# Kernel tuning notes

Hardware: AMD Instinct MI355X
Metric: run time of the kernel (lower is better)

## Reference

```python
import jax, jax.numpy as jnp
import numpy as np
from jax import lax

S = 2048      # services
MAXL = 16     # max exec steps per service
D = 4096      # devices
RN = 128      # size_realnode
HN = 128      # size_hypernode
HEADS = 4
CH = RN + HN  # 256
NRO = 256     # readout neurons
NITER = 3
NEG = 0.2     # leaky relu slope


def _gru(x, h, Wih, Whh, bih, bhh):
    # PyTorch GRU/GRUCell equations, gate order (r, z, n)
    gi = x @ Wih + bih
    gh = h @ Whh + bhh
    ir, iz, ig = jnp.split(gi, 3, axis=-1)
    hr, hz, hg = jnp.split(gh, 3, axis=-1)
    r = jax.nn.sigmoid(ir + hr)
    z = jax.nn.sigmoid(iz + hz)
    n = jnp.tanh(ig + r * hg)
    return (1.0 - z) * n + z * h


def _mlp(x, W1, b1, W2, b2, W3, b3):
    # Linear-ReLU-(Dropout eval=id)-Linear-ReLU-Linear
    h = jax.nn.relu(x @ W1 + b1)
    h = jax.nn.relu(h @ W2 + b2)
    return h @ W3 + b3


def forward(realnode, arr, exeSeqs, index_devices, index_fragments, frag2dev_node, frag2dev_row, lengths, frag_service, frag_pos,
            W_dev, b_dev, W_frg, b_frg, W_srv, b_srv,
            C_Wih, C_Whh, C_bih, C_bhh, F_Wih, F_Whh, F_bih, F_bhh, D_Wih, D_Whh, D_bih, D_bhh,
            W_src, b_src, W_tgt, b_tgt, att, bias_att,
            Wt1, bt1, Wt2, bt2, Wt3, bt3, Wl1, bl1, Wl2, bl2, Wl3, bl3):
    nodes = realnode.shape[0] + 1          # row 0 is zero-pad row (1-based node ids)
    Sn, L2 = exeSeqs.shape
    L = L2 // 2
    Dn = index_devices.shape[0]
    dtype = realnode.dtype

    # initial real-node states (scatter with disjoint indices == set)
    devs = realnode[index_devices - 1] @ W_dev + b_dev
    frags = realnode[index_fragments - 1] @ W_frg + b_frg
    state = jnp.zeros((nodes, RN), dtype).at[index_devices].set(devs).at[index_fragments].set(frags)

    h_srv = arr @ W_srv + b_srv            # [S, HN] GRU hidden (torch shape [1,S,HN])
    frag_state = state[index_fragments]

    for _ in range(NITER):
        # phiC: packed GRU over per-service execution sequences
        seq = state[exeSeqs].reshape(Sn, L, 2 * RN)   # [S, L, 2*RN]

        def step(h, xt_t):
            xt, t = xt_t
            hn = _gru(xt, h, C_Wih, C_Whh, C_bih, C_bhh)
            h = jnp.where((t < lengths)[:, None], hn, h)  # packed semantics: freeze past length
            return h, h

        h_srv, outs = lax.scan(step, h_srv, (seq.transpose(1, 0, 2), jnp.arange(L)))
        outs = outs.transpose(1, 0, 2)                # [S, L, HN]
        out_f = outs[frag_service, frag_pos]          # [F, HN] valid steps only (extract_indices)

        # messageF: hypernode output || state of device hosting the fragment
        msgF = jnp.concatenate([out_f, state[frag2dev_node]], axis=-1)   # [F, HN+RN]
        frag_state = state[index_fragments]
        frag_old = frag_state
        frag_state = _gru(msgF, frag_state, F_Wih, F_Whh, F_bih, F_bhh)

        # GAT-style scatter softmax over devices
        src = (jnp.concatenate([out_f, frag_old], axis=-1) @ W_src + b_src).reshape(-1, HEADS, CH)  # [F,H,CH]
        dev_state = state[index_devices]
        tgt = (dev_state @ W_tgt + b_tgt).reshape(-1, HEADS, CH)                                    # [D,H,CH]
        e = jax.nn.leaky_relu(src + tgt[frag2dev_row], NEG)
        alpha = (e * att).sum(-1)                                        # [F, HEADS]
        amax = jax.ops.segment_max(alpha, frag2dev_row, num_segments=Dn)
        w = jnp.exp(alpha - amax[frag2dev_row])
        wsum = jax.ops.segment_sum(w, frag2dev_row, num_segments=Dn)
        a = w / (wsum[frag2dev_row] + 1e-16)
        msgD = jax.ops.segment_sum(src * a[:, :, None], frag2dev_row, num_segments=Dn)
        msgD = msgD.mean(axis=1) + bias_att                              # [D, CH]
        dev_state = _gru(msgD, dev_state, D_Wih, D_Whh, D_bih, D_bhh)

        state = jnp.zeros((nodes, RN), dtype).at[index_devices].set(dev_state).at[index_fragments].set(frag_state)

    # mean-pool fragment states per service
    pooled = jax.ops.segment_sum(frag_state, frag_service, num_segments=Sn) / lengths[:, None].astype(dtype)
    latency = _mlp(pooled, Wl1, bl1, Wl2, bl2, Wl3, bl3)[:, 0]           # [S]
    thr = _mlp(h_srv, Wt1, bt1, Wt2, bt2, Wt3, bt3)[:, 0]                # [S]
    return jnp.concatenate([latency, thr])[None, :]                      # [1, 2S]


def setup_inputs() -> dict:
    lengths_np = np.tile(np.array([4, 8, 12, 16], dtype=np.int64), S // 4)
    F = int(lengths_np.sum())            # 20480 fragments
    num_real = D + F                     # 24576
    rng = np.random.RandomState(0)
    frag2dev_row = rng.randint(0, D, size=F).astype(np.int64)       # device row per fragment
    frag_service = np.repeat(np.arange(S, dtype=np.int64), lengths_np)
    frag_pos = np.concatenate([np.arange(l, dtype=np.int64) for l in lengths_np])
    index_devices = np.arange(1, D + 1, dtype=np.int64)             # 1-based node ids
    index_fragments = np.arange(D + 1, D + F + 1, dtype=np.int64)
    dev_node = frag2dev_row + 1
    exeSeqs = np.zeros((S, 2 * MAXL), dtype=np.int64)               # pad with 0 (zero row)
    exeSeqs[frag_service, 2 * frag_pos] = index_fragments
    exeSeqs[frag_service, 2 * frag_pos + 1] = dev_node

    keys = iter(jax.random.split(jax.random.key(0), 64))
    def rn(shape, s=0.05):
        return jax.random.normal(next(keys), shape, jnp.float32) * s
    z = lambda *sh: jnp.zeros(sh, jnp.float32)

    return {
        'realnode': rn((num_real, 5), 1.0), 'arr': rn((S, 5), 1.0),
        'exeSeqs': jnp.asarray(exeSeqs), 'index_devices': jnp.asarray(index_devices),
        'index_fragments': jnp.asarray(index_fragments), 'frag2dev_node': jnp.asarray(dev_node),
        'frag2dev_row': jnp.asarray(frag2dev_row), 'lengths': jnp.asarray(lengths_np),
        'frag_service': jnp.asarray(frag_service), 'frag_pos': jnp.asarray(frag_pos),
        'W_dev': rn((5, RN), 0.3), 'b_dev': z(RN), 'W_frg': rn((5, RN), 0.3), 'b_frg': z(RN),
        'W_srv': rn((5, HN), 0.3), 'b_srv': z(HN),
        'C_Wih': rn((2 * RN, 3 * HN)), 'C_Whh': rn((HN, 3 * HN)), 'C_bih': z(3 * HN), 'C_bhh': z(3 * HN),
        'F_Wih': rn((CH, 3 * RN)), 'F_Whh': rn((RN, 3 * RN)), 'F_bih': z(3 * RN), 'F_bhh': z(3 * RN),
        'D_Wih': rn((CH, 3 * RN)), 'D_Whh': rn((RN, 3 * RN)), 'D_bih': z(3 * RN), 'D_bhh': z(3 * RN),
        'W_src': rn((CH, HEADS * CH)), 'b_src': z(HEADS * CH),
        'W_tgt': rn((RN, HEADS * CH)), 'b_tgt': z(HEADS * CH),
        'att': rn((1, HEADS, CH), 0.1), 'bias_att': z(CH),
        'Wt1': rn((HN, NRO)), 'bt1': z(NRO), 'Wt2': rn((NRO, NRO)), 'bt2': z(NRO), 'Wt3': rn((NRO, 1)), 'bt3': z(1),
        'Wl1': rn((RN, NRO)), 'bl1': z(NRO), 'Wl2': rn((NRO, NRO)), 'bl2': z(NRO), 'Wl3': rn((NRO, 1)), 'bl3': z(1),
    }


def reference(realnode, arr, exeSeqs, index_devices, index_fragments, frag2dev_node, frag2dev_row, lengths, frag_service, frag_pos,
              W_dev, b_dev, W_frg, b_frg, W_srv, b_srv,
              C_Wih, C_Whh, C_bih, C_bhh, F_Wih, F_Whh, F_bih, F_bhh, D_Wih, D_Whh, D_bih, D_bhh,
              W_src, b_src, W_tgt, b_tgt, att, bias_att,
              Wt1, bt1, Wt2, bt2, Wt3, bt3, Wl1, bl1, Wl2, bl2, Wl3, bl3):
    return forward(realnode, arr, exeSeqs, index_devices, index_fragments, frag2dev_node, frag2dev_row, lengths, frag_service, frag_pos,
                   W_dev, b_dev, W_frg, b_frg, W_srv, b_srv,
                   C_Wih, C_Whh, C_bih, C_bhh, F_Wih, F_Whh, F_bih, F_bhh, D_Wih, D_Whh, D_bih, D_bhh,
                   W_src, b_src, W_tgt, b_tgt, att, bias_att,
                   Wt1, bt1, Wt2, bt2, Wt3, bt3, Wl1, bl1, Wl2, bl2, Wl3, bl3)
```

## Files before the change

kernel.cpp:

```cpp
#include <hip/hip_runtime.h>
#include <hip/hip_bf16.h>

typedef __attribute__((ext_vector_type(8))) short bf16x8;
typedef __attribute__((ext_vector_type(4))) float f32x4;

__device__ __forceinline__ float sigf(float x){ return 1.0f/(1.0f+expf(-x)); }
__device__ __forceinline__ int clampi(int v, int lo, int hi){ return v<lo?lo:(v>hi?hi:v); }
__device__ __forceinline__ unsigned short f2b(float f){
    __hip_bfloat16 h = __float2bfloat16(f);
    return *reinterpret_cast<unsigned short*>(&h);
}
__device__ __forceinline__ float us2f(unsigned short u){ return __uint_as_float(((unsigned)u)<<16); }

__device__ __forceinline__ void gload16(const void* g, void* l){
    __builtin_amdgcn_global_load_lds((const __attribute__((address_space(1))) void*)g,
                                     (__attribute__((address_space(3))) void*)l, 16, 0, 0);
}

__global__ void k_cvt(const int* __restrict__ src, int* __restrict__ dst, int n,
                      const int* __restrict__ det)
{
    int i = blockIdx.x*blockDim.x + threadIdx.x;
    if (i >= n) return;
    int stride = (det[1] == 0) ? 2 : 1;
    dst[i] = src[(size_t)i*stride];
}

__global__ void k_wt(const float* __restrict__ W, unsigned short* __restrict__ Wt,
                     int N, int kshift, int kmask, int total)
{
    int idx = blockIdx.x*blockDim.x + threadIdx.x;
    if (idx >= total) return;
    int n = idx >> kshift, k = idx & kmask;
    Wt[idx] = f2b(W[(size_t)k*N + n]);
}

__global__ void k_wt2(const float* __restrict__ W, unsigned short* __restrict__ Whi,
                      unsigned short* __restrict__ Wlo, int N, int kshift, int kmask, int total)
{
    int idx = blockIdx.x*blockDim.x + threadIdx.x;
    if (idx >= total) return;
    int n = idx >> kshift, k = idx & kmask;
    float v = W[(size_t)k*N + n];
    unsigned short hi = f2b(v);
    Whi[idx] = hi;
    Wlo[idx] = f2b(v - us2f(hi));
}

__global__ void k_proj5(const float* __restrict__ X, const float* __restrict__ W,
                        const float* __restrict__ bias,
                        const int* __restrict__ gidx, const int* __restrict__ sidx,
                        float* __restrict__ out, unsigned short* __restrict__ outBf,
                        float* __restrict__ out2, unsigned short* __restrict__ out2Bf,
                        int M, int nrows, int nodes)
{
    int t = blockIdx.x*blockDim.x + threadIdx.x;
    int i = t >> 7, j = t & 127;
    if (i >= M) return;
    int src = gidx ? clampi(gidx[i]-1, 0, nrows-1) : i;
    const float* xp = X + (size_t)src*5;
    float acc = bias[j];
#pragma unroll
    for (int k=0;k<5;k++) acc += xp[k] * W[k*128+j];
    int dr = sidx ? clampi(sidx[i], 0, nodes-1) : i;
    if (out)   out[(size_t)dr*128 + j] = acc;
    if (outBf) outBf[(size_t)dr*128 + j] = f2b(acc);
    if (out2)  out2[(size_t)i*128 + j] = acc;
    if (out2Bf) out2Bf[(size_t)i*128 + j] = f2b(acc);
}

__launch_bounds__(256)
__global__ void k_mm(const float* __restrict__ A0, int lda,
                     const float* __restrict__ B, int ldb,
                     const float* __restrict__ bias, float* __restrict__ C,
                     int M, int N, int K, int relu, float scale, int accum)
{
    __shared__ float As[16][132];
    __shared__ float Bs[16][132];
    int tid = threadIdx.x;
    int tx = tid & 15, ty = tid >> 4;
    int row0 = blockIdx.y * 128, col0 = blockIdx.x * 128;
    float acc[8][8] = {};
    for (int k0 = 0; k0 < K; k0 += 16){
#pragma unroll
        for (int q = 0; q < 2; ++q){
            int idx = tid + q*256;
            int r = idx >> 2, k4 = (idx & 3) * 4;
            const float* src = A0 + (size_t)(row0+r)*lda + k0 + k4;
            float4 v = *reinterpret_cast<const float4*>(src);
            As[k4+0][r]=v.x; As[k4+1][r]=v.y; As[k4+2][r]=v.z; As[k4+3][r]=v.w;
        }
#pragma unroll
        for (int q = 0; q < 2; ++q){
            int idx = tid + q*256;
            int kb = idx >> 5, n4 = (idx & 31) * 4;
            float4 v = *reinterpret_cast<const float4*>(B + (size_t)(k0+kb)*ldb + col0 + n4);
            *reinterpret_cast<float4*>(&Bs[kb][n4]) = v;
        }
        __syncthreads();
#pragma unroll
        for (int k = 0; k < 16; ++k){
            float a[8], b[8];
            *(float4*)&a[0] = *(const float4*)&As[k][ty*8];
            *(float4*)&a[4] = *(const float4*)&As[k][ty*8+4];
            *(float4*)&b[0] = *(const float4*)&Bs[k][tx*8];
            *(float4*)&b[4] = *(const float4*)&Bs[k][tx*8+4];
#pragma unroll
            for (int i=0;i<8;i++)
#pragma unroll
                for (int j=0;j<8;j++) acc[i][j] += a[i]*b[j];
        }
        __syncthreads();
    }
    float bb[8];
#pragma unroll
    for (int j=0;j<8;j++) bb[j] = bias ? bias[col0+tx*8+j] : 0.f;
#pragma unroll
    for (int i=0;i<8;i++){
        float* cp = C + (size_t)(row0+ty*8+i)*N + col0 + tx*8;
#pragma unroll
        for (int jq=0;jq<2;jq++){
            float4 prev = accum ? *(const float4*)(cp+jq*4) : make_float4(0,0,0,0);
            float o[4];
#pragma unroll
            for (int c=0;c<4;c++){
                float u = acc[i][jq*4+c] + bb[jq*4+c];
                if (relu) u = fmaxf(u,0.f);
                o[c] = (&prev.x)[c] + scale*u;
            }
            *(float4*)(cp+jq*4) = make_float4(o[0],o[1],o[2],o[3]);
        }
    }
}

struct MJob {
    const unsigned short *A0, *A1;
    const int *i0, *i1;
    const unsigned short *Wt;
    const float *bias;
    void *C;
    int N, K, epi, nrow;
    float scale;
};

#define MM2_SMEM 67840

__device__ __forceinline__ void mm2_body(const MJob J, int bid, char* smem)
{
    unsigned short* AsB = (unsigned short*)smem;
    unsigned short* BsB = AsB + 16384;
    int tid = threadIdx.x;
    int l = tid & 63, w = tid >> 6;
    int wr = w >> 1, wc = w & 1;
    int row0 = (bid % J.nrow) * 128, col0 = (bid / J.nrow) * 128;
    int nK = J.K >> 6;

    f32x4 acc[4][4];
#pragma unroll
    for (int m=0;m<4;m++)
#pragma unroll
        for (int n=0;n<4;n++) acc[m][n] = (f32x4){0.f,0.f,0.f,0.f};

    auto stage = [&](int buf, int k0){
        unsigned short* As = AsB + buf*8192;
        unsigned short* Bs = BsB + buf*8192;
#pragma unroll
        for (int q=0;q<4;q++){
            int slot = q*256 + w*64 + l;
            int r = slot >> 3, c8 = slot & 7;
            int g8 = c8 ^ (r & 7);
            int row; const unsigned short* base; int kl;
            if (k0 < 128){ row = J.i0 ? J.i0[row0+r] : (row0+r); base = J.A0; kl = k0; }
            else         { row = J.i1 ? J.i1[row0+r] : (row0+r); base = J.A1; kl = k0-128; }
            const char* g = (const char*)(base + (size_t)row*128 + kl) + g8*16;
            gload16(g, (void*)&As[(size_t)(q*256 + w*64)*8]);
        }
#pragma unroll
        for (int q=0;q<4;q++){
            int slot = q*256 + w*64 + l;
            int n = slot >> 3, kc = slot & 7;
            int g8 = kc ^ (n & 7);
            const char* g = (const char*)(J.Wt + (size_t)(col0+n)*J.K + k0) + g8*16;
            gload16(g, (void*)&Bs[(size_t)(q*256 + w*64)*8]);
        }
    };

    stage(0, 0);
    __syncthreads();
    for (int ks=0; ks<nK; ++ks){
        int cur = ks & 1;
        if (ks+1 < nK) stage(cur^1, (ks+1)*64);
        unsigned short* As = AsB + cur*8192;
        unsigned short* Bs = BsB + cur*8192;
#pragma unroll
        for (int kk = 0; kk < 2; ++kk){
            int ek = kk*32 + (l >> 4) * 8;
            bf16x8 af[4], bf[4];
#pragma unroll
            for (int m=0;m<4;m++){
                int r = wr*64 + m*16 + (l & 15);
                af[m] = *reinterpret_cast<const bf16x8*>(&As[r*64 + (ek ^ ((r & 7) << 3))]);
            }
#pragma unroll
            for (int n=0;n<4;n++){
                int c = wc*64 + n*16 + (l & 15);
                bf[n] = *reinterpret_cast<const bf16x8*>(&Bs[c*64 + (ek ^ ((c & 7) << 3))]);
            }
#pragma unroll
            for (int m=0;m<4;m++)
#pragma unroll
                for (int n=0;n<4;n++)
                    acc[m][n] = __builtin_amdgcn_mfma_f32_16x16x32_bf16(af[m], bf[n], acc[m][n], 0, 0, 0);
        }
        __syncthreads();
    }

    if (J.epi == 0){
        float* Ct = (float*)smem;
#pragma unroll
        for (int m=0;m<4;m++){
#pragma unroll
            for (int v=0;v<4;v++){
                int rl = wr*64 + m*16 + (l >> 4)*4 + v;
#pragma unroll
                for (int n=0;n<4;n++){
                    int c = wc*64 + n*16 + (l & 15);
                    Ct[rl*132 + c] = J.scale*acc[m][n][v] + (J.bias ? J.bias[col0+c] : 0.f);
                }
            }
        }
        __syncthreads();
#pragma unroll
        for (int q=0;q<16;q++){
            int idx = tid + q*256;
            int r = idx >> 5, c4 = (idx & 31)*4;
            float4 v = *reinterpret_cast<const float4*>(&Ct[r*132 + c4]);
            *reinterpret_cast<float4*>((float*)J.C + (size_t)(row0+r)*J.N + col0 + c4) = v;
        }
    } else {
        unsigned short* Cb = (unsigned short*)smem;
#pragma unroll
        for (int m=0;m<4;m++){
#pragma unroll
            for (int v=0;v<4;v++){
                int rl = wr*64 + m*16 + (l >> 4)*4 + v;
#pragma unroll
                for (int n=0;n<4;n++){
                    int c = wc*64 + n*16 + (l & 15);
                    Cb[rl*136 + c] = f2b(J.scale*acc[m][n][v] + (J.bias ? J.bias[col0+c] : 0.f));
                }
            }
        }
        __syncthreads();
#pragma unroll
        for (int q=0;q<8;q++){
            int idx = tid + q*256;
            int r = idx >> 4, c8 = (idx & 15)*8;
            uint4 v = *reinterpret_cast<const uint4*>(&Cb[r*136 + c8]);
            *reinterpret_cast<uint4*>((unsigned short*)J.C + (size_t)(row0+r)*J.N + col0 + c8) = v;
        }
    }
}

__launch_bounds__(256)
__global__ void mm2one(MJob a)
{
    __shared__ alignas(16) char smem[MM2_SMEM];
    mm2_body(a, blockIdx.x, smem);
}

__launch_bounds__(256)
__global__ void mm2two(MJob a, MJob b, int asplit)
{
    __shared__ alignas(16) char smem[MM2_SMEM];
    int bid = blockIdx.x;
    if (bid < asplit) mm2_body(a, bid, smem);
    else              mm2_body(b, bid - asplit, smem);
}

struct GJob {
    const unsigned short *A0, *A1;
    const int *i0, *i1;
    int lda;
    const unsigned short *Wih, *Whh;
    const float *bih, *bhh;
    float *H;
    unsigned short *Hbf, *stateBf;
    const int *sidx;
    int M, nodes;
};

__device__ __forceinline__ void gru_body(const GJob J, int bid, unsigned short* AsB, unsigned short* BsB)
{
    int tid = threadIdx.x;
    int l = tid & 63, w = tid >> 6;
    int row0 = bid * 128;
    f32x4 acc[24], accN[8];
#pragma unroll
    for (int n=0;n<24;n++) acc[n] = (f32x4){0.f,0.f,0.f,0.f};
#pragma unroll
    for (int n=0;n<8;n++) accN[n] = (f32x4){0.f,0.f,0.f,0.f};

    auto stage = [&](int buf, int st){
        int k0 = st*64;
        unsigned short* As = AsB + buf*8192;
        unsigned short* Bs = BsB + buf*24576;
#pragma unroll
        for (int q=0;q<2;q++){
            int slot = q*512 + w*64 + l;
            int r = slot >> 3, c8 = slot & 7;
            int g8 = c8 ^ (r & 7);
            const unsigned short* src;
            if (st < 4){
                if (J.i1){
                    if (k0 < 128){ int ri = J.i0 ? J.i0[row0+r] : (row0+r); src = J.A0 + (size_t)ri*128 + k0; }
                    else         { int ri = J.i1[row0+r]; src = J.A1 + (size_t)ri*128 + (k0-128); }
                } else {
                    src = J.A0 + (size_t)(row0+r)*J.lda + k0;
                }
            } else {
                src = J.Hbf + (size_t)(row0+r)*128 + (k0-256);
            }
            gload16((const char*)src + g8*16, (void*)&As[(size_t)(q*512 + w*64)*8]);
        }
#pragma unroll
        for (int q=0;q<6;q++){
            int slot = q*512 + w*64 + l;
            int n = slot >> 3, kc = slot & 7;
            int g8 = kc ^ (n & 7);
            const unsigned short* src = (st < 4) ? (J.Wih + (size_t)n*256 + k0)
                                                 : (J.Whh + (size_t)n*128 + (k0-256));
            gload16((const char*)src + g8*16, (void*)&Bs[(size_t)(q*512 + w*64)*8]);
        }
    };

    stage(0, 0);
    __syncthreads();
    for (int st=0; st<4; ++st){
        int cur = st & 1;
        stage(cur^1, st+1);
        unsigned short* As = AsB + cur*8192;
        unsigned short* Bs = BsB + cur*24576;
#pragma unroll
        for (int kk=0; kk<2; ++kk){
            int ek = kk*32 + (l >> 4)*8;
            int r = w*16 + (l & 15);
            bf16x8 af = *reinterpret_cast<const bf16x8*>(&As[r*64 + (ek ^ ((r & 7) << 3))]);
#pragma unroll
            for (int n=0;n<24;n++){
                int c = n*16 + (l & 15);
                bf16x8 bf = *reinterpret_cast<const bf16x8*>(&Bs[c*64 + (ek ^ ((c & 7) << 3))]);
                acc[n] = __builtin_amdgcn_mfma_f32_16x16x32_bf16(af, bf, acc[n], 0, 0, 0);
            }
        }
        __syncthreads();
    }
    for (int st=4; st<6; ++st){
        int cur = st & 1;
        if (st+1 < 6) stage(cur^1, st+1);
        unsigned short* As = AsB + cur*8192;
        unsigned short* Bs = BsB + cur*24576;
#pragma unroll
        for (int kk=0; kk<2; ++kk){
            int ek = kk*32 + (l >> 4)*8;
            int r = w*16 + (l & 15);
            bf16x8 af = *reinterpret_cast<const bf16x8*>(&As[r*64 + (ek ^ ((r & 7) << 3))]);
#pragma unroll
            for (int n=0;n<24;n++){
                int c = n*16 + (l & 15);
                bf16x8 bf = *reinterpret_cast<const bf16x8*>(&Bs[c*64 + (ek ^ ((c & 7) << 3))]);
                if (n < 16) acc[n]     = __builtin_amdgcn_mfma_f32_16x16x32_bf16(af, bf, acc[n], 0, 0, 0);
                else        accN[n-16] = __builtin_amdgcn_mfma_f32_16x16x32_bf16(af, bf, accN[n-16], 0, 0, 0);
            }
        }
        __syncthreads();
    }
#pragma unroll
    for (int v=0;v<4;v++){
        int row = row0 + w*16 + (l >> 4)*4 + v;
        int st = clampi(J.sidx[row],0,J.nodes-1);
#pragma unroll
        for (int c=0;c<8;c++){
            int col = c*16 + (l & 15);
            float rr = sigf(acc[c][v]    + J.bih[col]     + J.bhh[col]);
            float zz = sigf(acc[c+8][v]  + J.bih[col+128] + J.bhh[col+128]);
            float nn = tanhf(acc[c+16][v] + J.bih[col+256] + rr*(accN[c][v] + J.bhh[col+256]));
            float hv = J.H[(size_t)row*128 + col];
            float hn = (1.f-zz)*nn + zz*hv;
            unsigned short hb = f2b(hn);
            J.H[(size_t)row*128 + col] = hn;
            J.Hbf[(size_t)row*128 + col] = hb;
            J.stateBf[(size_t)st*128 + col] = hb;
        }
    }
}

__launch_bounds__(512)
__global__ void gru2(GJob a, GJob b, int asplit)
{
    __shared__ alignas(16) unsigned short AsB[2*8192];
    __shared__ alignas(16) unsigned short BsB[2*24576];
    int bid = blockIdx.x;
    if (bid < asplit) gru_body(a, bid, AsB, BsB);
    else              gru_body(b, bid - asplit, AsB, BsB);
}

__launch_bounds__(256)
__global__ void k_attn(const unsigned short* __restrict__ SRC, const unsigned short* __restrict__ tgtbf,
                       const float* __restrict__ att, const int* __restrict__ list,
                       const int* __restrict__ offs, const float* __restrict__ batt,
                       unsigned short* __restrict__ msgDbf,
                       float* __restrict__ alphaG, int Dn, int F)
{
    __shared__ float tg[1024];
    __shared__ float alds[128*4];
    __shared__ float accs[4][256];
    int d = blockIdx.x;
    int tid = threadIdx.x;
    int w = tid >> 6, lane = tid & 63;
    for (int u = tid; u < 1024; u += 256) tg[u] = us2f(tgtbf[(size_t)d*1024 + u]);
    __syncthreads();
    int beg = offs[d], end = offs[d+1];
    if (beg < 0) beg = 0; if (end > F) end = F; if (end < beg) end = beg;
    int c0 = w*256 + lane*4;
    float t0 = tg[c0], t1 = tg[c0+1], t2 = tg[c0+2], t3 = tg[c0+3];
    float a0 = att[c0], a1 = att[c0+1], a2 = att[c0+2], a3 = att[c0+3];
    float amax = -3.4e38f;
    for (int i=beg;i<end;i++){
        int f = list[i];
        ushort4 sv = *reinterpret_cast<const ushort4*>(SRC + (size_t)f*1024 + c0);
        float e0 = us2f(sv.x)+t0, e1 = us2f(sv.y)+t1, e2 = us2f(sv.z)+t2, e3 = us2f(sv.w)+t3;
        e0 = e0>0.f?e0:0.2f*e0; e1 = e1>0.f?e1:0.2f*e1;
        e2 = e2>0.f?e2:0.2f*e2; e3 = e3>0.f?e3:0.2f*e3;
        float s = e0*a0 + e1*a1 + e2*a2 + e3*a3;
#pragma unroll
        for (int msk=1; msk<64; msk<<=1) s += __shfl_xor(s, msk);
        int li = i - beg;
        if (li < 128){ if (lane == 0) alds[li*4+w] = s; }
        else         { if (lane == 0) alphaG[(size_t)f*4+w] = s; }
        amax = fmaxf(amax, s);
    }
    __syncthreads();
    float wsum = 0.f;
    for (int i=beg;i<end;i++){
        int li = i - beg;
        float a = (li < 128) ? alds[li*4+w] : alphaG[(size_t)list[i]*4+w];
        wsum += expf(a - amax);
    }
    float iws = 1.f/(wsum + 1e-16f);
    float acc[4] = {0,0,0,0};
    for (int i=beg;i<end;i++){
        int f = list[i];
        int li = i - beg;
        float a = (li < 128) ? alds[li*4+w] : alphaG[(size_t)f*4+w];
        float p = expf(a - amax)*iws;
        ushort4 sv = *reinterpret_cast<const ushort4*>(SRC + (size_t)f*1024 + c0);
        acc[0] += p*us2f(sv.x); acc[1] += p*us2f(sv.y);
        acc[2] += p*us2f(sv.z); acc[3] += p*us2f(sv.w);
    }
#pragma unroll
    for (int j=0;j<4;j++) accs[w][lane*4+j] = acc[j];
    __syncthreads();
    if (tid < 256){
        float m = (accs[0][tid]+accs[1][tid]+accs[2][tid]+accs[3][tid])*0.25f + batt[tid];
        msgDbf[(size_t)d*256 + tid] = f2b(m);
    }
}

__launch_bounds__(512)
__global__ void k_recur(float* __restrict__ h_srv, const float* __restrict__ giF,
                        const unsigned short* __restrict__ Whi,
                        const unsigned short* __restrict__ Wlo,
                        const float* __restrict__ bhh,
                        const int* __restrict__ inv,
                        unsigned short* __restrict__ out_f_bf,
                        int S, int L, int F)
{
    __shared__ float hs[16][129];
    __shared__ alignas(16) unsigned short hsHi[16*128];
    __shared__ alignas(16) unsigned short hsLo[16*128];
    __shared__ float ghs[16][385];
    __shared__ int fLoc[16][16];
    int tid = threadIdx.x;
    int l = tid & 63, w = tid >> 6;
    int lane15 = l & 15, lhi = l >> 4;
    int s0 = blockIdx.x * 16;
    for (int u = tid; u < 2048; u += 512){
        int s=u>>7,k=u&127;
        float v = h_srv[(size_t)(s0+s)*128+k];
        hs[s][k] = v;
        unsigned short hb = f2b(v);
        int ksw = k ^ ((s & 7) << 3);
        hsHi[s*128 + ksw] = hb;
        hsLo[s*128 + ksw] = f2b(v - us2f(hb));
    }
    if (tid < 256) fLoc[tid>>4][tid&15] = inv[(size_t)(s0+(tid&15))*L + (tid>>4)];
    bf16x8 wHi[3][4], wLo[3][4];
#pragma unroll
    for (int ct=0; ct<3; ++ct){
        int col = w*48 + ct*16 + lane15;
#pragma unroll
        for (int ks=0; ks<4; ++ks){
            size_t off = (size_t)col*128 + ks*32 + lhi*8;
            wHi[ct][ks] = *reinterpret_cast<const bf16x8*>(Whi + off);
            wLo[ct][ks] = *reinterpret_cast<const bf16x8*>(Wlo + off);
        }
    }
    __syncthreads();
    for (int t=0;t<L;++t){
        bf16x8 hHi[4], hLo[4];
#pragma unroll
        for (int ks=0; ks<4; ++ks){
            int ek = ks*32 + lhi*8;
            int off = lane15*128 + (ek ^ ((lane15 & 7) << 3));
            hHi[ks] = *reinterpret_cast<const bf16x8*>(&hsHi[off]);
            hLo[ks] = *reinterpret_cast<const bf16x8*>(&hsLo[off]);
        }
#pragma unroll
        for (int ct=0; ct<3; ++ct){
            f32x4 acc = (f32x4){0.f,0.f,0.f,0.f};
#pragma unroll
            for (int ks=0; ks<4; ++ks){
                acc = __builtin_amdgcn_mfma_f32_16x16x32_bf16(hHi[ks], wHi[ct][ks], acc, 0,0,0);
                acc = __builtin_amdgcn_mfma_f32_16x16x32_bf16(hLo[ks], wHi[ct][ks], acc, 0,0,0);
                acc = __builtin_amdgcn_mfma_f32_16x16x32_bf16(hHi[ks], wLo[ct][ks], acc, 0,0,0);
            }
            int col = w*48 + ct*16 + lane15;
            float bb = bhh[col];
#pragma unroll
            for (int v=0; v<4; ++v){
                ghs[lhi*4 + v][col] = acc[v] + bb;
            }
        }
        __syncthreads();
        for (int u = tid; u < 2048; u += 512){
            int s=u>>7, k=u&127; int f = fLoc[t][s];
            if (f >= 0 && f < F){
                const float* gp = giF + (size_t)f*384;
                float r  = sigf(gp[k]     + ghs[s][k]);
                float zz = sigf(gp[128+k] + ghs[s][128+k]);
                float n  = tanhf(gp[256+k] + r*ghs[s][256+k]);
                float hn = (1.f-zz)*n + zz*hs[s][k];
                hs[s][k] = hn;
                unsigned short hb = f2b(hn);
                int ksw = k ^ ((s & 7) << 3);
                hsHi[s*128 + ksw] = hb;
                hsLo[s*128 + ksw] = f2b(hn - us2f(hb));
                out_f_bf[(size_t)f*128+k] = hb;
            }
        }
        __syncthreads();
    }
    for (int u = tid; u < 2048; u += 512){ int s=u>>7,k=u&127; h_srv[(size_t)(s0+s)*128+k] = hs[s][k]; }
}

__global__ void k_count(const int* __restrict__ row, int* __restrict__ counts, int F, int Dn)
{ int f = blockIdx.x*blockDim.x + threadIdx.x; if (f < F) atomicAdd(&counts[clampi(row[f],0,Dn-1)], 1); }

__global__ void k_scan(const int* __restrict__ counts, int* __restrict__ offs, int D)
{
    __shared__ int part[257];
    int tid = threadIdx.x;
    int per = (D + 255) / 256;
    int s = 0;
    for (int i=0;i<per;i++){ int idx = tid*per+i; if (idx < D) s += counts[idx]; }
    part[tid] = s;
    __syncthreads();
    if (tid == 0){
        int acc = 0;
        for (int i=0;i<256;i++){ int v = part[i]; part[i] = acc; acc += v; }
        part[256] = acc;
    }
    __syncthreads();
    int acc = part[tid];
    for (int i=0;i<per;i++){ int idx = tid*per+i; if (idx < D){ offs[idx] = acc; acc += counts[idx]; } }
    if (tid == 0) offs[D] = part[256];
}

__global__ void k_fill(const int* __restrict__ row, const int* __restrict__ offs,
                       int* __restrict__ cursor, int* __restrict__ list, int F, int Dn)
{
    int f = blockIdx.x*blockDim.x + threadIdx.x;
    if (f >= F) return;
    int r = clampi(row[f],0,Dn-1);
    int p = atomicAdd(&cursor[r], 1);
    int pos = offs[r]+p;
    if (pos >= 0 && pos < F) list[pos] = f;
}

__global__ void k_build_inv(const int* __restrict__ fs, const int* __restrict__ fp,
                            int* __restrict__ inv, int F, int L, int S)
{
    int f = blockIdx.x*blockDim.x + threadIdx.x;
    if (f >= F) return;
    inv[clampi(fs[f],0,S-1)*L + clampi(fp[f],0,L-1)] = f;
}

__global__ void k_pool_add(const float* __restrict__ frag, const int* __restrict__ fs,
                           float* __restrict__ pooled, int F, int S)
{
    int t = blockIdx.x*blockDim.x + threadIdx.x;
    int i = t >> 7, j = t & 127;
    if (i >= F) return;
    atomicAdd(&pooled[(size_t)clampi(fs[i],0,S-1)*128 + j], frag[(size_t)i*128 + j]);
}

__global__ void k_pool_div(float* __restrict__ pooled, const int* __restrict__ lengths, int S)
{
    int t = blockIdx.x*blockDim.x + threadIdx.x;
    int i = t >> 7, j = t & 127;
    if (i >= S) return;
    int l = lengths[i]; if (l < 1) l = 1;
    pooled[(size_t)i*128 + j] /= (float)l;
}

__global__ void k_dot_out(const float* __restrict__ H, const float* __restrict__ W3,
                          const float* __restrict__ b3, float* __restrict__ outv, int off)
{
    __shared__ float red[256];
    int s = blockIdx.x, tid = threadIdx.x;
    red[tid] = H[(size_t)s*256 + tid] * W3[tid];
    __syncthreads();
    for (int st=128; st; st>>=1){ if (tid < st) red[tid] += red[tid+st]; __syncthreads(); }
    if (tid == 0) outv[off + s] = red[0] + b3[0];
}

extern "C" void kernel_launch(void* const* d_in, const int* in_sizes, int n_in,
                              void* d_out, int out_size, void* d_ws, size_t ws_size,
                              hipStream_t stream)
{
    (void)n_in; (void)out_size; (void)ws_size;
    const float* realnode = (const float*)d_in[0];
    const float* arr      = (const float*)d_in[1];
    const int* r_exe   = (const int*)d_in[2];
    const int* r_idev  = (const int*)d_in[3];
    const int* r_ifrag = (const int*)d_in[4];
    const int* r_fdn   = (const int*)d_in[5];
    const int* r_fdr   = (const int*)d_in[6];
    const int* r_len   = (const int*)d_in[7];
    const int* r_fsvc  = (const int*)d_in[8];
    const int* r_fpos  = (const int*)d_in[9];
    const float *W_dev=(const float*)d_in[10], *b_dev=(const float*)d_in[11];
    const float *W_frg=(const float*)d_in[12], *b_frg=(const float*)d_in[13];
    const float *W_srv=(const float*)d_in[14], *b_srv=(const float*)d_in[15];
    const float *C_Wih=(const float*)d_in[16], *C_Whh=(const float*)d_in[17], *C_bih=(const float*)d_in[18], *C_bhh=(const float*)d_in[19];
    const float *F_Wih=(const float*)d_in[20], *F_Whh=(const float*)d_in[21], *F_bih=(const float*)d_in[22], *F_bhh=(const float*)d_in[23];
    const float *D_Wih=(const float*)d_in[24], *D_Whh=(const float*)d_in[25], *D_bih=(const float*)d_in[26], *D_bhh=(const float*)d_in[27];
    const float *W_src=(const float*)d_in[28], *b_src=(const float*)d_in[29];
    const float *W_tgt=(const float*)d_in[30], *b_tgt=(const float*)d_in[31];
    const float *att=(const float*)d_in[32], *bias_att=(const float*)d_in[33];
    const float *Wt1=(const float*)d_in[34], *bt1=(const float*)d_in[35], *Wt2=(const float*)d_in[36], *bt2=(const float*)d_in[37], *Wt3=(const float*)d_in[38], *bt3=(const float*)d_in[39];
    const float *Wl1=(const float*)d_in[40], *bl1=(const float*)d_in[41], *Wl2=(const float*)d_in[42], *bl2=(const float*)d_in[43], *Wl3=(const float*)d_in[44], *bl3=(const float*)d_in[45];
    float* outp = (float*)d_out;

    const int S  = in_sizes[7];
    const int Dn = in_sizes[3];
    const int F  = in_sizes[4];
    const int L  = in_sizes[2] / (2*S);
    const int nreal = in_sizes[0]/5;
    const int nodes = nreal + 1;
    const int NIT = 3;

    char* wp = (char*)d_ws;
    auto alloc = [&](size_t nelem)->float*{
        float* p = (float*)wp;
        wp += ((nelem*4 + 255)/256)*256;
        return p;
    };
    float* h_srv  = alloc((size_t)S*128);
    float* fragA  = alloc((size_t)F*128);
    float* devA   = alloc((size_t)Dn*128);
    float* alphaB = alloc((size_t)F*4);
    float* UNION  = alloc((size_t)F*512);
    float* giF    = UNION;
    unsigned short* SRC = (unsigned short*)UNION;
    float* Z      = alloc((size_t)Dn*1024);
    float* TGTf   = alloc((size_t)Dn*512);
    unsigned short* TGT = (unsigned short*)TGTf;
    float* pooled = alloc((size_t)S*128);
    unsigned short* state_bf = (unsigned short*)alloc((size_t)nodes*64);
    unsigned short* out_f_bf = (unsigned short*)alloc((size_t)F*64);
    unsigned short* fragA_bf = (unsigned short*)alloc((size_t)F*64);
    unsigned short* devA_bf  = (unsigned short*)alloc((size_t)Dn*64);
    unsigned short* msgD_bf  = (unsigned short*)alloc((size_t)Dn*128);
    unsigned short* tCWih   = (unsigned short*)alloc(384*256/2);
    unsigned short* tCWhhHi = (unsigned short*)alloc(384*128/2);
    unsigned short* tCWhhLo = (unsigned short*)alloc(384*128/2);
    unsigned short* tFWih   = (unsigned short*)alloc(384*256/2);
    unsigned short* tFWhh   = (unsigned short*)alloc(384*128/2);
    unsigned short* tDWih   = (unsigned short*)alloc(384*256/2);
    unsigned short* tDWhh   = (unsigned short*)alloc(384*128/2);
    unsigned short* tWtgt   = (unsigned short*)alloc(1024*128/2);
    unsigned short* tWsrc   = (unsigned short*)alloc(1024*256/2);
    int* cExe   = (int*)alloc((size_t)S*2*L);
    int* cIdev  = (int*)alloc((size_t)Dn);
    int* cIfrag = (int*)alloc((size_t)F);
    int* cFdn   = (int*)alloc((size_t)F);
    int* cFdr   = (int*)alloc((size_t)F);
    int* cLen   = (int*)alloc((size_t)S);
    int* cFsvc  = (int*)alloc((size_t)F);
    int* cFpos  = (int*)alloc((size_t)F);
    int* inv    = (int*)alloc((size_t)S*L);
    int* counts = (int*)alloc((size_t)Dn);
    int* offs   = (int*)alloc((size_t)Dn+1);
    int* cursor = (int*)alloc((size_t)Dn);
    int* list   = (int*)alloc((size_t)F);

    const int* det = r_idev;
    auto cvt = [&](const int* src, int* dst, int n){
        k_cvt<<<dim3((n+255)/256),256,0,stream>>>(src, dst, n, det);
    };
    cvt(r_exe,  cExe,  S*2*L);
    cvt(r_idev, cIdev, Dn);
    cvt(r_ifrag,cIfrag,F);
    cvt(r_fdn,  cFdn,  F);
    cvt(r_fdr,  cFdr,  F);
    cvt(r_len,  cLen,  S);
    cvt(r_fsvc, cFsvc, F);
    cvt(r_fpos, cFpos, F);

    k_wt<<<dim3((98304+255)/256),256,0,stream>>>(C_Wih, tCWih, 384, 8, 255, 98304);
    k_wt2<<<dim3((49152+255)/256),256,0,stream>>>(C_Whh, tCWhhHi, tCWhhLo, 384, 7, 127, 49152);
    k_wt<<<dim3((98304+255)/256),256,0,stream>>>(F_Wih, tFWih, 384, 8, 255, 98304);
    k_wt<<<dim3((49152+255)/256),256,0,stream>>>(F_Whh, tFWhh, 384, 7, 127, 49152);
    k_wt<<<dim3((98304+255)/256),256,0,stream>>>(D_Wih, tDWih, 384, 8, 255, 98304);
    k_wt<<<dim3((49152+255)/256),256,0,stream>>>(D_Whh, tDWhh, 384, 7, 127, 49152);
    k_wt<<<dim3((131072+255)/256),256,0,stream>>>(W_tgt, tWtgt, 1024, 7, 127, 131072);
    k_wt<<<dim3((262144+255)/256),256,0,stream>>>(W_src, tWsrc, 1024, 8, 255, 262144);

    hipMemsetAsync(state_bf, 0, (size_t)nodes*128*2, stream);
    hipMemsetAsync(inv, 0xFF, (size_t)S*L*4, stream);
    hipMemsetAsync(counts, 0, (size_t)Dn*4, stream);
    hipMemsetAsync(cursor, 0, (size_t)Dn*4, stream);

    k_proj5<<<dim3((Dn*128+255)/256),256,0,stream>>>(realnode, W_dev, b_dev, cIdev, cIdev,
        nullptr, state_bf, devA, devA_bf, Dn, nreal, nodes);
    k_proj5<<<dim3(((size_t)F*128+255)/256),256,0,stream>>>(realnode, W_frg, b_frg, cIfrag, cIfrag,
        nullptr, state_bf, fragA, fragA_bf, F, nreal, nodes);
    k_proj5<<<dim3((S*128+255)/256),256,0,stream>>>(arr, W_srv, b_srv, nullptr, nullptr,
        h_srv, nullptr, nullptr, nullptr, S, S, nodes);
    k_build_inv<<<dim3((F+255)/256),256,0,stream>>>(cFsvc, cFpos, inv, F, L, S);
    k_count<<<dim3((F+255)/256),256,0,stream>>>(cFdr, counts, F, Dn);
    k_scan<<<1,256,0,stream>>>(counts, offs, Dn);
    k_fill<<<dim3((F+255)/256),256,0,stream>>>(cFdr, offs, cursor, list, F, Dn);

    const int nrF = F/128, nrD = Dn/128;
    MJob jGi  = { state_bf, state_bf, cIfrag, cFdn, tCWih, C_bih, giF, 384, 256, 0, nrF, 1.f };
    MJob jTgt = { devA_bf, devA_bf, nullptr, nullptr, tWtgt, b_tgt, TGT, 1024, 128, 2, nrD, 1.f };
    MJob jSrc = { out_f_bf, fragA_bf, nullptr, nullptr, tWsrc, b_src, SRC, 1024, 256, 2, nrF, 1.f };
    GJob jF = { out_f_bf, state_bf, nullptr, cFdn, 128, tFWih, tFWhh, F_bih, F_bhh,
                fragA, fragA_bf, state_bf, cIfrag, F, nodes };
    GJob jD = { msgD_bf, nullptr, nullptr, nullptr, 256, tDWih, tDWhh, D_bih, D_bhh,
                devA, devA_bf, state_bf, cIdev, Dn, nodes };

    for (int it=0; it<NIT; ++it){
        mm2two<<<dim3(3*nrF + 8*nrD),256,0,stream>>>(jGi, jTgt, 3*nrF);
        k_recur<<<dim3(S/16),512,0,stream>>>(h_srv, giF, tCWhhHi, tCWhhLo, C_bhh, inv,
            out_f_bf, S, L, F);
        mm2one<<<dim3(8*nrF),256,0,stream>>>(jSrc);
        k_attn<<<dim3(Dn),256,0,stream>>>(SRC, TGT, att, list, offs, bias_att,
            msgD_bf, alphaB, Dn, F);
        gru2<<<dim3(nrF + nrD),512,0,stream>>>(jF, jD, nrF);
    }

    hipMemsetAsync(pooled, 0, (size_t)S*128*4, stream);
    k_pool_add<<<dim3(((size_t)F*128+255)/256),256,0,stream>>>(fragA, cFsvc, pooled, F, S);
    k_pool_div<<<dim3((S*128+255)/256),256,0,stream>>>(pooled, cLen, S);
    float* h1 = (float*)TGTf;
    k_mm<<<dim3(256/128, S/128),256,0,stream>>>(pooled, 128, Wl1, 256, bl1, h1, S, 256, 128, 1, 1.f, 0);
    k_mm<<<dim3(256/128, S/128),256,0,stream>>>(h1, 256, Wl2, 256, bl2, Z, S, 256, 256, 1, 1.f, 0);
    k_dot_out<<<dim3(S),256,0,stream>>>(Z, Wl3, bl3, outp, 0);
    k_mm<<<dim3(256/128, S/128),256,0,stream>>>(h_srv, 128, Wt1, 256, bt1, h1, S, 256, 128, 1, 1.f, 0);
    k_mm<<<dim3(256/128, S/128),256,0,stream>>>(h1, 256, Wt2, 256, bt2, Z, S, 256, 256, 1, 1.f, 0);
    k_dot_out<<<dim3(S),256,0,stream>>>(Z, Wt3, bt3, outp, S);
}
```

Before: 859.6 us.

## Pipeline GEMM staging with partial vmcnt waits, halve recur block size, bf16 gi

The GEMM and GRU kernels now use explicit s_waitcnt vmcnt with raw barriers instead of __syncthreads, so the next stage's async LDS loads can stay in flight while the current tile is computed. The two GRU stage loops are merged into one. The recurrent kernel handles 8 services per block instead of 16, doubling the grid for the sequential scan. The gi projection is stored in bf16, which halves its memory traffic at some cost in precision. The vmcnt(8) count assumes a fixed number of outstanding loads per stage, and half of the padded MFMA rows in k_recur now do no useful work.

```diff
diff --git a/kernel.cpp b/kernel.cpp
--- a/kernel.cpp
+++ b/kernel.cpp
@@ -186,10 +186,16 @@
     };
 
     stage(0, 0);
-    __syncthreads();
     for (int ks=0; ks<nK; ++ks){
         int cur = ks & 1;
-        if (ks+1 < nK) stage(cur^1, (ks+1)*64);
+        if (ks+1 < nK){
+            stage(cur^1, (ks+1)*64);
+            asm volatile("s_waitcnt vmcnt(8)" ::: "memory");
+        } else {
+            asm volatile("s_waitcnt vmcnt(0)" ::: "memory");
+        }
+        __builtin_amdgcn_s_barrier();
+        __builtin_amdgcn_sched_barrier(0);
         unsigned short* As = AsB + cur*8192;
         unsigned short* Bs = BsB + cur*8192;
 #pragma unroll
@@ -212,7 +218,8 @@
                 for (int n=0;n<4;n++)
                     acc[m][n] = __builtin_amdgcn_mfma_f32_16x16x32_bf16(af[m], bf[n], acc[m][n], 0, 0, 0);
         }
-        __syncthreads();
+        __builtin_amdgcn_sched_barrier(0);
+        __builtin_amdgcn_s_barrier();
     }
 
     if (J.epi == 0){
@@ -335,45 +342,48 @@
     };
 
     stage(0, 0);
-    __syncthreads();
-    for (int st=0; st<4; ++st){
+    for (int st=0; st<6; ++st){
         int cur = st & 1;
-        stage(cur^1, st+1);
+        if (st+1 < 6){
+            stage(cur^1, st+1);
+            asm volatile("s_waitcnt vmcnt(8)" ::: "memory");
+        } else {
+            asm volatile("s_waitcnt vmcnt(0)" ::: "memory");
+        }
+        __builtin_amdgcn_s_barrier();
+        __builtin_amdgcn_sched_barrier(0);
         unsigned short* As = AsB + cur*8192;
         unsigned short* Bs = BsB + cur*24576;
-#pragma unroll
-        for (int kk=0; kk<2; ++kk){
-            int ek = kk*32 + (l >> 4)*8;
-            int r = w*16 + (l & 15);
-            bf16x8 af = *reinterpret_cast<const bf16x8*>(&As[r*64 + (ek ^ ((r & 7) << 3))]);
-#pragma unroll
-            for (int n=0;n<24;n++){
-                int c = n*16 + (l & 15);
-                bf16x8 bf = *reinterpret_cast<const bf16x8*>(&Bs[c*64 + (ek ^ ((c & 7) << 3))]);
-                acc[n] = __builtin_amdgcn_mfma_f32_16x16x32_bf16(af, bf, acc[n], 0, 0, 0);
-            }
-        }
-        __syncthreads();
-    }
-    for (int st=4; st<6; ++st){
-        int cur = st & 1;
-        if (st+1 < 6) stage(cur^1, st+1);
-        unsigned short* As = AsB + cur*8192;
-        unsigned short* Bs = BsB + cur*24576;
-#pragma unroll
-        for (int kk=0; kk<2; ++kk){
-            int ek = kk*32 + (l >> 4)*8;
-            int r = w*16 + (l & 15);
-            bf16x8 af = *reinterpret_cast<const bf16x8*>(&As[r*64 + (ek ^ ((r & 7) << 3))]);
-#pragma unroll
-            for (int n=0;n<24;n++){
-                int c = n*16 + (l & 15);
-                bf16x8 bf = *reinterpret_cast<const bf16x8*>(&Bs[c*64 + (ek ^ ((c & 7) << 3))]);
-                if (n < 16) acc[n]     = __builtin_amdgcn_mfma_f32_16x16x32_bf16(af, bf, acc[n], 0, 0, 0);
-                else        accN[n-16] = __builtin_amdgcn_mfma_f32_16x16x32_bf16(af, bf, accN[n-16], 0, 0, 0);
-            }
-        }
-        __syncthreads();
+        if (st < 4){
+#pragma unroll
+            for (int kk=0; kk<2; ++kk){
+                int ek = kk*32 + (l >> 4)*8;
+                int r = w*16 + (l & 15);
+                bf16x8 af = *reinterpret_cast<const bf16x8*>(&As[r*64 + (ek ^ ((r & 7) << 3))]);
+#pragma unroll
+                for (int n=0;n<24;n++){
+                    int c = n*16 + (l & 15);
+                    bf16x8 bf = *reinterpret_cast<const bf16x8*>(&Bs[c*64 + (ek ^ ((c & 7) << 3))]);
+                    acc[n] = __builtin_amdgcn_mfma_f32_16x16x32_bf16(af, bf, acc[n], 0, 0, 0);
+                }
+            }
+        } else {
+#pragma unroll
+            for (int kk=0; kk<2; ++kk){
+                int ek = kk*32 + (l >> 4)*8;
+                int r = w*16 + (l & 15);
+                bf16x8 af = *reinterpret_cast<const bf16x8*>(&As[r*64 + (ek ^ ((r & 7) << 3))]);
+#pragma unroll
+                for (int n=0;n<24;n++){
+                    int c = n*16 + (l & 15);
+                    bf16x8 bf = *reinterpret_cast<const bf16x8*>(&Bs[c*64 + (ek ^ ((c & 7) << 3))]);
+                    if (n < 16) acc[n]     = __builtin_amdgcn_mfma_f32_16x16x32_bf16(af, bf, acc[n], 0, 0, 0);
+                    else        accN[n-16] = __builtin_amdgcn_mfma_f32_16x16x32_bf16(af, bf, accN[n-16], 0, 0, 0);
+                }
+            }
+        }
+        __builtin_amdgcn_sched_barrier(0);
+        __builtin_amdgcn_s_barrier();
     }
 #pragma unroll
     for (int v=0;v<4;v++){
@@ -468,7 +478,7 @@
 }
 
 __launch_bounds__(512)
-__global__ void k_recur(float* __restrict__ h_srv, const float* __restrict__ giF,
+__global__ void k_recur(float* __restrict__ h_srv, const unsigned short* __restrict__ giFb,
                         const unsigned short* __restrict__ Whi,
                         const unsigned short* __restrict__ Wlo,
                         const float* __restrict__ bhh,
@@ -476,25 +486,30 @@
                         unsigned short* __restrict__ out_f_bf,
                         int S, int L, int F)
 {
-    __shared__ float hs[16][129];
+    __shared__ float hs[8][129];
     __shared__ alignas(16) unsigned short hsHi[16*128];
     __shared__ alignas(16) unsigned short hsLo[16*128];
     __shared__ float ghs[16][385];
-    __shared__ int fLoc[16][16];
+    __shared__ int fLoc[16][8];
     int tid = threadIdx.x;
     int l = tid & 63, w = tid >> 6;
     int lane15 = l & 15, lhi = l >> 4;
-    int s0 = blockIdx.x * 16;
+    int s0 = blockIdx.x * 8;
     for (int u = tid; u < 2048; u += 512){
         int s=u>>7,k=u&127;
-        float v = h_srv[(size_t)(s0+s)*128+k];
-        hs[s][k] = v;
-        unsigned short hb = f2b(v);
         int ksw = k ^ ((s & 7) << 3);
-        hsHi[s*128 + ksw] = hb;
-        hsLo[s*128 + ksw] = f2b(v - us2f(hb));
-    }
-    if (tid < 256) fLoc[tid>>4][tid&15] = inv[(size_t)(s0+(tid&15))*L + (tid>>4)];
+        if (s < 8){
+            float v = h_srv[(size_t)(s0+s)*128+k];
+            hs[s][k] = v;
+            unsigned short hb = f2b(v);
+            hsHi[s*128 + ksw] = hb;
+            hsLo[s*128 + ksw] = f2b(v - us2f(hb));
+        } else {
+            hsHi[s*128 + ksw] = 0;
+            hsLo[s*128 + ksw] = 0;
+        }
+    }
+    if (tid < 128) fLoc[tid>>3][tid&7] = inv[(size_t)(s0+(tid&7))*L + (tid>>3)];
     bf16x8 wHi[3][4], wLo[3][4];
 #pragma unroll
     for (int ct=0; ct<3; ++ct){
@@ -533,13 +548,13 @@
             }
         }
         __syncthreads();
-        for (int u = tid; u < 2048; u += 512){
+        for (int u = tid; u < 1024; u += 512){
             int s=u>>7, k=u&127; int f = fLoc[t][s];
             if (f >= 0 && f < F){
-                const float* gp = giF + (size_t)f*384;
-                float r  = sigf(gp[k]     + ghs[s][k]);
-                float zz = sigf(gp[128+k] + ghs[s][128+k]);
-                float n  = tanhf(gp[256+k] + r*ghs[s][256+k]);
+                const unsigned short* gp = giFb + (size_t)f*384;
+                float r  = sigf(us2f(gp[k])     + ghs[s][k]);
+                float zz = sigf(us2f(gp[128+k]) + ghs[s][128+k]);
+                float n  = tanhf(us2f(gp[256+k]) + r*ghs[s][256+k]);
                 float hn = (1.f-zz)*n + zz*hs[s][k];
                 hs[s][k] = hn;
                 unsigned short hb = f2b(hn);
@@ -551,7 +566,7 @@
         }
         __syncthreads();
     }
-    for (int u = tid; u < 2048; u += 512){ int s=u>>7,k=u&127; h_srv[(size_t)(s0+s)*128+k] = hs[s][k]; }
+    for (int u = tid; u < 1024; u += 512){ int s=u>>7,k=u&127; h_srv[(size_t)(s0+s)*128+k] = hs[s][k]; }
 }
 
 __global__ void k_count(const int* __restrict__ row, int* __restrict__ counts, int F, int Dn)
@@ -672,8 +687,8 @@
     float* devA   = alloc((size_t)Dn*128);
     float* alphaB = alloc((size_t)F*4);
     float* UNION  = alloc((size_t)F*512);
-    float* giF    = UNION;
-    unsigned short* SRC = (unsigned short*)UNION;
+    unsigned short* giFb = (unsigned short*)UNION;
+    unsigned short* SRC  = (unsigned short*)UNION;
     float* Z      = alloc((size_t)Dn*1024);
     float* TGTf   = alloc((size_t)Dn*512);
     unsigned short* TGT = (unsigned short*)TGTf;
@@ -745,7 +760,7 @@
     k_fill<<<dim3((F+255)/256),256,0,stream>>>(cFdr, offs, cursor, list, F, Dn);
 
     const int nrF = F/128, nrD = Dn/128;
-    MJob jGi  = { state_bf, state_bf, cIfrag, cFdn, tCWih, C_bih, giF, 384, 256, 0, nrF, 1.f };
+    MJob jGi  = { state_bf, state_bf, cIfrag, cFdn, tCWih, C_bih, giFb, 384, 256, 2, nrF, 1.f };
     MJob jTgt = { devA_bf, devA_bf, nullptr, nullptr, tWtgt, b_tgt, TGT, 1024, 128, 2, nrD, 1.f };
     MJob jSrc = { out_f_bf, fragA_bf, nullptr, nullptr, tWsrc, b_src, SRC, 1024, 256, 2, nrF, 1.f };
     GJob jF = { out_f_bf, state_bf, nullptr, cFdn, 128, tFWih, tFWhh, F_bih, F_bhh,
@@ -755,7 +770,7 @@
 
     for (int it=0; it<NIT; ++it){
         mm2two<<<dim3(3*nrF + 8*nrD),256,0,stream>>>(jGi, jTgt, 3*nrF);
-        k_recur<<<dim3(S/16),512,0,stream>>>(h_srv, giF, tCWhhHi, tCWhhLo, C_bhh, inv,
+        k_recur<<<dim3(S/8),512,0,stream>>>(h_srv, giFb, tCWhhHi, tCWhhLo, C_bhh, inv,
             out_f_bf, S, L, F);
         mm2one<<<dim3(8*nrF),256,0,stream>>>(jSrc);
         k_attn<<<dim3(Dn),256,0,stream>>>(SRC, TGT, att, list, offs, bias_att,
```

Result: faster. 801.8 us (-6.7%).
